# Kernel tuning notes

Hardware: AMD Instinct MI355X
Metric: run time of the kernel (lower is better)

Reference implementation:

```python
import jax, jax.numpy as jnp
import numpy as np

N = 50000      # nodes
H = 128        # hidden_size
RBF = 20       # edge_embedding_size
E_CHE = 400000 # chemical edges
E_VDW = 200000 # van-der-Waals edges


def _prelu(x, a):
    return jnp.where(x > 0, x, a * x)


def _mlp(x, w1, b1, a1, w2, b2, a2):
    # Linear -> PReLU -> Linear -> PReLU (PaiNN message / filter MLP)
    h = _prelu(x @ w1 + b1, a1)
    return _prelu(h @ w2 + b2, a2)


def setup_inputs() -> dict:
    key = jax.random.key(0)
    ks = list(jax.random.split(key, 64))
    it = iter(ks)
    d = {}
    d['node_scalar'] = jax.random.normal(next(it), (N, H), jnp.float32)
    d['node_vector'] = jax.random.normal(next(it), (N, 3, H), jnp.float32)
    for pfx, E in (('che', E_CHE), ('vdw', E_VDW)):
        d[pfx + '_edge'] = jax.random.randint(next(it), (E, 2), 0, N)
        d[pfx + '_edge_diff'] = jax.random.normal(next(it), (E, 3), jnp.float32)
        d[pfx + '_edge_dist'] = jax.random.uniform(next(it), (E,), jnp.float32) + 0.5  # strictly positive
        d[pfx + '_rbf_dist'] = jax.random.normal(next(it), (E, RBF), jnp.float32)
    # four 2-layer MLPs with per-layer PReLU scalar slope (torch default init 0.25)
    def mlp_params(pfx, din):
        s1 = 1.0 / np.sqrt(din)
        s2 = 1.0 / np.sqrt(H)
        d[pfx + '_w1'] = jax.random.uniform(next(it), (din, H), jnp.float32, -s1, s1)
        d[pfx + '_b1'] = jax.random.uniform(next(it), (H,), jnp.float32, -s1, s1)
        d[pfx + '_a1'] = jnp.asarray(0.25, jnp.float32)
        d[pfx + '_w2'] = jax.random.uniform(next(it), (H, 3 * H), jnp.float32, -s2, s2)
        d[pfx + '_b2'] = jax.random.uniform(next(it), (3 * H,), jnp.float32, -s2, s2)
        d[pfx + '_a2'] = jnp.asarray(0.25, jnp.float32)
    mlp_params('che_s', H)    # che scalar message MLP
    mlp_params('che_f', RBF)  # che filter layer
    mlp_params('vdw_s', H)
    mlp_params('vdw_f', RBF)
    return d


def _branch(node_scalar, node_vector, edge, edge_diff, edge_dist, rbf, sp, fp):
    # sp/fp: 6-tuples of MLP params. edge[:,1]=source gather, edge[:,0]=dest scatter.
    scalar_out = _mlp(node_scalar, *sp)          # [N, 3H]
    filter_w = _mlp(rbf, *fp)                    # [E, 3H]
    filter_out = scalar_out[edge[:, 1]] * filter_w  # gather + gate
    gate_vector, message_scalar, gate_edge = jnp.split(filter_out, 3, axis=1)
    state_vector = node_vector[edge[:, 1]] * gate_vector[:, None, :]        # [E,3,H]
    unit = edge_diff / edge_dist[:, None]                                    # [E,3]
    edge_vector = unit[:, :, None] * gate_edge[:, None, :]                   # [E,3,H]
    message_vector = state_vector + edge_vector
    res_scalar = jax.ops.segment_sum(message_scalar, edge[:, 0], num_segments=N)
    res_vector = jax.ops.segment_sum(message_vector, edge[:, 0], num_segments=N)
    return res_scalar, res_vector


def reference(node_scalar, node_vector,
              che_edge, che_edge_diff, che_edge_dist, che_rbf_dist,
              vdw_edge, vdw_edge_diff, vdw_edge_dist, vdw_rbf_dist,
              che_s_w1, che_s_b1, che_s_a1, che_s_w2, che_s_b2, che_s_a2,
              che_f_w1, che_f_b1, che_f_a1, che_f_w2, che_f_b2, che_f_a2,
              vdw_s_w1, vdw_s_b1, vdw_s_a1, vdw_s_w2, vdw_s_b2, vdw_s_a2,
              vdw_f_w1, vdw_f_b1, vdw_f_a1, vdw_f_w2, vdw_f_b2, vdw_f_a2):
    che_sp = (che_s_w1, che_s_b1, che_s_a1, che_s_w2, che_s_b2, che_s_a2)
    che_fp = (che_f_w1, che_f_b1, che_f_a1, che_f_w2, che_f_b2, che_f_a2)
    vdw_sp = (vdw_s_w1, vdw_s_b1, vdw_s_a1, vdw_s_w2, vdw_s_b2, vdw_s_a2)
    vdw_fp = (vdw_f_w1, vdw_f_b1, vdw_f_a1, vdw_f_w2, vdw_f_b2, vdw_f_a2)
    che_rs, che_rv = _branch(node_scalar, node_vector, che_edge, che_edge_diff,
                             che_edge_dist, che_rbf_dist, che_sp, che_fp)
    vdw_rs, vdw_rv = _branch(node_scalar, node_vector, vdw_edge, vdw_edge_diff,
                             vdw_edge_dist, vdw_rbf_dist, vdw_sp, vdw_fp)
    return (node_scalar + che_rs + vdw_rs, node_vector + che_rv + vdw_rv)
```

## Files before the change

kernel.cpp:

```cpp
#include <hip/hip_runtime.h>
#include <hip/hip_bf16.h>

typedef float f32x4 __attribute__((ext_vector_type(4)));
typedef short bf16x8 __attribute__((ext_vector_type(8)));

#define HD 128
#define TILE 32
#define SCAN_TILE 2048

__device__ __forceinline__ float prelu_f(float x, float a) {
  return x > 0.f ? x : a * x;
}

__device__ __forceinline__ unsigned short f2bf(float x) {
  __hip_bfloat16 h = __float2bfloat16(x);
  return *reinterpret_cast<unsigned short*>(&h);
}
__device__ __forceinline__ float bf2f(unsigned short u) {
  union { unsigned u; float f; } a; a.u = ((unsigned)u) << 16;
  return a.f;
}
__device__ __forceinline__ f32x4 bf4_to_f32(ushort4 u) {
  f32x4 r; r[0] = bf2f(u.x); r[1] = bf2f(u.y); r[2] = bf2f(u.z); r[3] = bf2f(u.w);
  return r;
}

__global__ __launch_bounds__(256) void init_conv_kernel(
    const f32x4* __restrict__ ns, const f32x4* __restrict__ nv,
    f32x4* __restrict__ out, ushort4* __restrict__ ns_bf, ushort4* __restrict__ nv_bf,
    int n_ns4, int n_nv4)
{
  int total = n_ns4 + n_nv4;
  for (int i = blockIdx.x * 256 + threadIdx.x; i < total; i += gridDim.x * 256) {
    f32x4 v = (i < n_ns4) ? ns[i] : nv[i - n_ns4];
    out[i] = v;
    ushort4 o;
    o.x = f2bf(v[0]); o.y = f2bf(v[1]); o.z = f2bf(v[2]); o.w = f2bf(v[3]);
    if (i < n_ns4) ns_bf[i] = o; else nv_bf[i - n_ns4] = o;
  }
}

__global__ __launch_bounds__(256) void weights_prep_kernel(
    const float* __restrict__ w2s_che, const float* __restrict__ w2f_che,
    const float* __restrict__ w2s_vdw, const float* __restrict__ w2f_vdw,
    const float* __restrict__ w1n_che, const float* __restrict__ w1n_vdw,
    const float* __restrict__ w1e_che, const float* __restrict__ w1e_vdw,
    unsigned short* __restrict__ d_w2t_sche, unsigned short* __restrict__ d_w2t_fche,
    unsigned short* __restrict__ d_w2t_svdw, unsigned short* __restrict__ d_w2t_fvdw,
    unsigned short* __restrict__ d_w1t_nche, unsigned short* __restrict__ d_w1t_nvdw,
    unsigned short* __restrict__ d_w1t_eche, unsigned short* __restrict__ d_w1t_evdw)
{
  int idx = blockIdx.x * 256 + threadIdx.x;
  if (idx < 4 * 49152) {
    int which = idx / 49152, rem = idx % 49152;
    int c = rem >> 7, k = rem & 127;
    const float* s = which == 0 ? w2s_che : which == 1 ? w2f_che : which == 2 ? w2s_vdw : w2f_vdw;
    unsigned short* d = which == 0 ? d_w2t_sche : which == 1 ? d_w2t_fche : which == 2 ? d_w2t_svdw : d_w2t_fvdw;
    d[rem] = f2bf(s[(size_t)k * 384 + c]);
  } else if (idx < 4 * 49152 + 2 * 16384) {
    int rem2 = idx - 4 * 49152;
    int which = rem2 / 16384, rem = rem2 % 16384;
    int c = rem >> 7, k = rem & 127;
    const float* s = which ? w1n_vdw : w1n_che;
    unsigned short* d = which ? d_w1t_nvdw : d_w1t_nche;
    d[rem] = f2bf(s[(size_t)k * 128 + c]);
  } else if (idx < 4 * 49152 + 2 * 16384 + 2 * 4096) {
    int rem2 = idx - 4 * 49152 - 2 * 16384;
    int which = rem2 / 4096, rem = rem2 % 4096;
    int c = rem >> 5, k = rem & 31;
    const float* s = which ? w1e_vdw : w1e_che;
    unsigned short* d = which ? d_w1t_evdw : d_w1t_eche;
    d[rem] = (k < 20) ? f2bf(s[(size_t)k * 128 + c]) : (unsigned short)0;
  }
}

__global__ __launch_bounds__(256) void node_mlp_mfma(
    const unsigned short* __restrict__ Abf,
    const unsigned short* __restrict__ w1t,
    const float* __restrict__ b1, const float* __restrict__ a1p,
    const unsigned short* __restrict__ w2t,
    const float* __restrict__ b2, const float* __restrict__ a2p,
    unsigned short* __restrict__ out,
    int M)
{
  __shared__ __attribute__((aligned(16))) unsigned short A_lds[64 * HD];
  __shared__ __attribute__((aligned(16))) unsigned short h_lds[64 * HD];
  const int t = threadIdx.x;
  const int wvid = t >> 6, lane = t & 63, l15 = lane & 15, l4 = lane >> 4;
  const int m0 = blockIdx.x * 64;
  const float a1 = a1p[0], a2 = a2p[0];

  for (int idx = t; idx < 64 * HD / 8; idx += 256) {
    int row = idx >> 4, seg = (idx & 15) * 8;
    bf16x8 v = 0;
    if (m0 + row < M) v = *(const bf16x8*)&Abf[(size_t)(m0 + row) * HD + seg];
    *(bf16x8*)&A_lds[row * HD + (seg ^ ((row & 7) << 3))] = v;
  }
  __syncthreads();

  {
    bf16x8 Bf[2][4];
    #pragma unroll
    for (int nf = 0; nf < 2; nf++)
      #pragma unroll
      for (int ks = 0; ks < 4; ks++) {
        int col = wvid * 32 + nf * 16 + l15;
        Bf[nf][ks] = *(const bf16x8*)&w1t[(size_t)col * 128 + ks * 32 + l4 * 8];
      }
    f32x4 D[4][2];
    #pragma unroll
    for (int mi = 0; mi < 4; mi++)
      #pragma unroll
      for (int nf = 0; nf < 2; nf++)
        #pragma unroll
        for (int cc = 0; cc < 4; cc++) D[mi][nf][cc] = 0.f;

    #pragma unroll
    for (int mi = 0; mi < 4; mi++)
      #pragma unroll
      for (int ks = 0; ks < 4; ks++) {
        int row = mi * 16 + l15;
        bf16x8 Af = *(const bf16x8*)&A_lds[row * HD + ((ks * 32 + l4 * 8) ^ ((row & 7) << 3))];
        D[mi][0] = __builtin_amdgcn_mfma_f32_16x16x32_bf16(Af, Bf[0][ks], D[mi][0], 0, 0, 0);
        D[mi][1] = __builtin_amdgcn_mfma_f32_16x16x32_bf16(Af, Bf[1][ks], D[mi][1], 0, 0, 0);
      }

    float b1v0 = b1[wvid * 32 + l15];
    float b1v1 = b1[wvid * 32 + 16 + l15];
    #pragma unroll
    for (int mi = 0; mi < 4; mi++)
      #pragma unroll
      for (int nf = 0; nf < 2; nf++)
        #pragma unroll
        for (int r4 = 0; r4 < 4; r4++) {
          int row = mi * 16 + l4 * 4 + r4;
          int col = wvid * 32 + nf * 16 + l15;
          h_lds[row * HD + (col ^ ((row & 7) << 3))] =
              f2bf(prelu_f(D[mi][nf][r4] + (nf ? b1v1 : b1v0), a1));
        }
  }
  __syncthreads();

  for (int m = 0; m < 3; m++) {
    bf16x8 Bf[2][4];
    #pragma unroll
    for (int nf = 0; nf < 2; nf++)
      #pragma unroll
      for (int ks = 0; ks < 4; ks++) {
        int col = m * 128 + wvid * 32 + nf * 16 + l15;
        Bf[nf][ks] = *(const bf16x8*)&w2t[(size_t)col * 128 + ks * 32 + l4 * 8];
      }
    f32x4 D[4][2];
    #pragma unroll
    for (int mi = 0; mi < 4; mi++)
      #pragma unroll
      for (int nf = 0; nf < 2; nf++)
        #pragma unroll
        for (int cc = 0; cc < 4; cc++) D[mi][nf][cc] = 0.f;

    #pragma unroll
    for (int mi = 0; mi < 4; mi++)
      #pragma unroll
      for (int ks = 0; ks < 4; ks++) {
        int row = mi * 16 + l15;
        bf16x8 Af = *(const bf16x8*)&h_lds[row * HD + ((ks * 32 + l4 * 8) ^ ((row & 7) << 3))];
        D[mi][0] = __builtin_amdgcn_mfma_f32_16x16x32_bf16(Af, Bf[0][ks], D[mi][0], 0, 0, 0);
        D[mi][1] = __builtin_amdgcn_mfma_f32_16x16x32_bf16(Af, Bf[1][ks], D[mi][1], 0, 0, 0);
      }

    float b2v0 = b2[m * 128 + wvid * 32 + l15];
    float b2v1 = b2[m * 128 + wvid * 32 + 16 + l15];
    #pragma unroll
    for (int mi = 0; mi < 4; mi++)
      #pragma unroll
      for (int nf = 0; nf < 2; nf++)
        #pragma unroll
        for (int r4 = 0; r4 < 4; r4++) {
          int row = mi * 16 + l4 * 4 + r4;
          if (m0 + row < M) {
            int col = m * 128 + wvid * 32 + nf * 16 + l15;
            out[(size_t)(m0 + row) * 384 + col] =
                f2bf(prelu_f(D[mi][nf][r4] + (nf ? b2v1 : b2v0), a2));
          }
        }
  }
}

__global__ __launch_bounds__(256) void zero_int_kernel(int* __restrict__ p, int n) {
  int i = blockIdx.x * 256 + threadIdx.x;
  if (i < n) p[i] = 0;
}

__global__ __launch_bounds__(256) void hist2_kernel(
    const int* __restrict__ edge_che, const int* __restrict__ edge_vdw,
    int* __restrict__ counts, int N, int E_che, int E_vdw)
{
  int g = blockIdx.x * 256 + threadIdx.x;
  if (g < E_che) {
    atomicAdd(&counts[edge_che[(size_t)g * 2]], 1);
  } else {
    int e2 = g - E_che;
    if (e2 < E_vdw) atomicAdd(&counts[N + edge_vdw[(size_t)e2 * 2]], 1);
  }
}

__global__ __launch_bounds__(256) void scan_partial2_kernel(
    const int* __restrict__ counts, int* __restrict__ partials, int n, int nb)
{
  const int b = blockIdx.x, t = threadIdx.x;
  const int br = b >= nb, lb = b - br * nb;
  const int* cnt = counts + (size_t)br * n;
  const int base = lb * SCAN_TILE + t * 8;
  int s = 0;
  #pragma unroll
  for (int i = 0; i < 8; i++) {
    int idx = base + i;
    if (idx < n) s += cnt[idx];
  }
  __shared__ int sums[256];
  sums[t] = s;
  __syncthreads();
  for (int o = 128; o > 0; o >>= 1) {
    if (t < o) sums[t] += sums[t + o];
    __syncthreads();
  }
  if (t == 0) partials[b] = sums[0];
}

__global__ __launch_bounds__(256) void scan_partials2_kernel(int* __restrict__ partials_g, int nb)
{
  int* partials = partials_g + blockIdx.x * nb;
  __shared__ int s[256];
  const int t = threadIdx.x;
  s[t] = (t < nb) ? partials[t] : 0;
  __syncthreads();
  for (int o = 1; o < 256; o <<= 1) {
    int v = s[t];
    int u = (t >= o) ? s[t - o] : 0;
    __syncthreads();
    s[t] = v + u;
    __syncthreads();
  }
  if (t < nb) partials[t] = (t == 0) ? 0 : s[t - 1];
}

__global__ __launch_bounds__(256) void scan_write2_kernel(
    const int* __restrict__ counts, const int* __restrict__ partials,
    int* __restrict__ offsets, int* __restrict__ cursor, int n, int nb,
    int E_che, int E_vdw)
{
  const int b = blockIdx.x, t = threadIdx.x;
  const int br = b >= nb, lb = b - br * nb;
  const int* cnt = counts + (size_t)br * n;
  int* offs = offsets + (size_t)br * (n + 1);
  int* curs = cursor + (size_t)br * n;
  const int base = lb * SCAN_TILE + t * 8;
  int vals[8];
  int s = 0;
  #pragma unroll
  for (int i = 0; i < 8; i++) {
    int idx = base + i;
    vals[i] = (idx < n) ? cnt[idx] : 0;
    s += vals[i];
  }
  __shared__ int sums[256];
  sums[t] = s;
  __syncthreads();
  for (int o = 1; o < 256; o <<= 1) {
    int v = sums[t];
    int u = (t >= o) ? sums[t - o] : 0;
    __syncthreads();
    sums[t] = v + u;
    __syncthreads();
  }
  int run = partials[b] + ((t == 0) ? 0 : sums[t - 1]);
  #pragma unroll
  for (int i = 0; i < 8; i++) {
    int idx = base + i;
    if (idx < n) {
      offs[idx] = run;
      curs[idx] = run;
      run += vals[i];
    }
  }
  if (lb == 0 && t == 0) offs[n] = br ? E_vdw : E_che;
}

__global__ __launch_bounds__(256) void scatter_ids2_kernel(
    const int* __restrict__ edge_che, const int* __restrict__ edge_vdw,
    int* __restrict__ cursor, int* __restrict__ edge_list,
    int N, int E_che, int E_vdw)
{
  int g = blockIdx.x * 256 + threadIdx.x;
  if (g < E_che) {
    int d = edge_che[(size_t)g * 2];
    int p = atomicAdd(&cursor[d], 1);
    edge_list[p] = g;
  } else {
    int e2 = g - E_che;
    if (e2 < E_vdw) {
      int d = edge_vdw[(size_t)e2 * 2];
      int p = atomicAdd(&cursor[N + d], 1);
      edge_list[E_che + p] = e2;
    }
  }
}

__global__ __launch_bounds__(256) void permute2_kernel(
    const int* __restrict__ edge_list,
    const int* __restrict__ edge_che, const float* __restrict__ diff_che,
    const float* __restrict__ dist_che, const float* __restrict__ rbf_che,
    const int* __restrict__ edge_vdw, const float* __restrict__ diff_vdw,
    const float* __restrict__ dist_vdw, const float* __restrict__ rbf_vdw,
    int* __restrict__ src_s, int* __restrict__ dst_s,
    float4* __restrict__ unit_s, unsigned short* __restrict__ rbf_b,
    int E_che, int E_vdw)
{
  int p = blockIdx.x * 256 + threadIdx.x;
  if (p >= E_che + E_vdw) return;
  int br = p >= E_che;
  int e = edge_list[p];
  const int* edge = br ? edge_vdw : edge_che;
  const float* diff = br ? diff_vdw : diff_che;
  const float* dist = br ? dist_vdw : dist_che;
  const float* rbf  = br ? rbf_vdw  : rbf_che;
  src_s[p] = edge[(size_t)e * 2 + 1];
  dst_s[p] = edge[(size_t)e * 2 + 0];
  float inv = 1.f / dist[e];
  float4 u;
  u.x = diff[(size_t)e * 3 + 0] * inv;
  u.y = diff[(size_t)e * 3 + 1] * inv;
  u.z = diff[(size_t)e * 3 + 2] * inv;
  u.w = 0.f;
  unit_s[p] = u;
  ushort4* ro = (ushort4*)(rbf_b + (size_t)p * 32);
  const float* rr = &rbf[(size_t)e * 20];
  #pragma unroll
  for (int i = 0; i < 5; i++) {
    ushort4 o;
    o.x = f2bf(rr[4 * i + 0]); o.y = f2bf(rr[4 * i + 1]);
    o.z = f2bf(rr[4 * i + 2]); o.w = f2bf(rr[4 * i + 3]);
    ro[i] = o;
  }
  ushort4 z; z.x = 0; z.y = 0; z.z = 0; z.w = 0;
  ro[5] = z; ro[6] = z; ro[7] = z;
}

__global__ __launch_bounds__(256, 4) void edge_mfma_reduce_kernel(
    const unsigned short* __restrict__ so,
    const unsigned short* __restrict__ nv,
    const int*   __restrict__ src_s,
    const int*   __restrict__ dst_s,
    const float4* __restrict__ unit_s,
    const unsigned short* __restrict__ rbf_b,
    const int*   __restrict__ offsets,
    const unsigned short* __restrict__ w1t,
    const float* __restrict__ b1, const float* __restrict__ a1p,
    const unsigned short* __restrict__ w2t,
    const float* __restrict__ b2, const float* __restrict__ a2p,
    float* __restrict__ out,
    int N, int E)
{
  __shared__ __attribute__((aligned(16))) unsigned short A1_lds[TILE * 40];
  __shared__ __attribute__((aligned(16))) unsigned short h_lds[TILE * HD];
  __shared__ __attribute__((aligned(16))) unsigned short P_lds[3][TILE * HD];
  __shared__ int src_l[TILE];
  __shared__ float unit_l[TILE][3];
  __shared__ int run_rs[TILE + 1], run_node[TILE], run_flag[TILE];
  __shared__ int nd_s;

  const int t = threadIdx.x;
  const int tx = t & 31, ty = t >> 5;
  const int c4 = tx * 4;
  const int wvid = t >> 6, lane = t & 63, l15 = lane & 15, l4 = lane >> 4;
  const int pblk = blockIdx.x * TILE;
  const int nrows = min(TILE, E - pblk);
  const float a1 = a1p[0], a2 = a2p[0];

  if (t < 64) {
    int d = -1, s = 0;
    float ux = 0.f, uy = 0.f, uz = 0.f;
    if (t < nrows) {
      s = src_s[pblk + t];
      d = dst_s[pblk + t];
      float4 u = unit_s[pblk + t];
      ux = u.x; uy = u.y; uz = u.z;
    }
    if (t < TILE) {
      src_l[t] = s;
      unit_l[t][0] = ux; unit_l[t][1] = uy; unit_l[t][2] = uz;
    }
    int dprev = __shfl_up(d, 1);
    bool flag = (t < nrows) && (t == 0 || d != dprev);
    unsigned long long mask = __ballot(flag ? 1 : 0);
    if (flag) {
      int j = __popcll(mask & ((1ull << t) - 1ull));
      run_rs[j] = t;
      run_node[j] = d;
      unsigned long long rest = (t == 63) ? 0ull : (mask >> (t + 1));
      int re = rest ? (t + 1 + (__ffsll((long long)rest) - 1)) : nrows;
      int interior = 1;
      if (t == 0 && offsets[d] != pblk) interior = 0;
      if (re == nrows && offsets[d + 1] != pblk + nrows) interior = 0;
      run_flag[j] = interior;
    }
    if (t == 0) {
      int nd = __popcll(mask);
      nd_s = nd;
      run_rs[nd] = nrows;
    }
  }

  if (t < TILE * 4) {
    const bf16x8* rb = (const bf16x8*)(rbf_b + (size_t)pblk * 32);
    int row = t >> 2, seg = (t & 3) * 8;
    *(bf16x8*)&A1_lds[row * 40 + seg] = rb[t];
  }
  __syncthreads();

  {
    bf16x8 B1[2];
    B1[0] = *(const bf16x8*)&w1t[(size_t)(wvid * 32 + l15) * 32 + l4 * 8];
    B1[1] = *(const bf16x8*)&w1t[(size_t)(wvid * 32 + 16 + l15) * 32 + l4 * 8];
    f32x4 D1[2][2];
    #pragma unroll
    for (int mi = 0; mi < 2; mi++)
      #pragma unroll
      for (int nf = 0; nf < 2; nf++)
        #pragma unroll
        for (int cc = 0; cc < 4; cc++) D1[mi][nf][cc] = 0.f;

    #pragma unroll
    for (int mi = 0; mi < 2; mi++) {
      bf16x8 Af = *(const bf16x8*)&A1_lds[(mi * 16 + l15) * 40 + l4 * 8];
      D1[mi][0] = __builtin_amdgcn_mfma_f32_16x16x32_bf16(Af, B1[0], D1[mi][0], 0, 0, 0);
      D1[mi][1] = __builtin_amdgcn_mfma_f32_16x16x32_bf16(Af, B1[1], D1[mi][1], 0, 0, 0);
    }

    float b1v0 = b1[wvid * 32 + l15];
    float b1v1 = b1[wvid * 32 + 16 + l15];
    #pragma unroll
    for (int mi = 0; mi < 2; mi++)
      #pragma unroll
      for (int nf = 0; nf < 2; nf++)
        #pragma unroll
        for (int r4 = 0; r4 < 4; r4++) {
          int row = mi * 16 + l4 * 4 + r4;
          int col = wvid * 32 + nf * 16 + l15;
          h_lds[row * HD + (col ^ ((row & 7) << 3))] =
              f2bf(prelu_f(D1[mi][nf][r4] + (nf ? b1v1 : b1v0), a1));
        }
  }
  __syncthreads();

  for (int m = 0; m < 3; m++) {
    bf16x8 Bf[2][4];
    #pragma unroll
    for (int nf = 0; nf < 2; nf++)
      #pragma unroll
      for (int ks = 0; ks < 4; ks++) {
        int col = m * 128 + wvid * 32 + nf * 16 + l15;
        Bf[nf][ks] = *(const bf16x8*)&w2t[(size_t)col * 128 + ks * 32 + l4 * 8];
      }
    f32x4 D[2][2];
    #pragma unroll
    for (int mi = 0; mi < 2; mi++)
      #pragma unroll
      for (int nf = 0; nf < 2; nf++)
        #pragma unroll
        for (int cc = 0; cc < 4; cc++) D[mi][nf][cc] = 0.f;

    #pragma unroll
    for (int mi = 0; mi < 2; mi++)
      #pragma unroll
      for (int ks = 0; ks < 4; ks++) {
        int row = mi * 16 + l15;
        bf16x8 Af = *(const bf16x8*)&h_lds[row * HD + ((ks * 32 + l4 * 8) ^ ((row & 7) << 3))];
        D[mi][0] = __builtin_amdgcn_mfma_f32_16x16x32_bf16(Af, Bf[0][ks], D[mi][0], 0, 0, 0);
        D[mi][1] = __builtin_amdgcn_mfma_f32_16x16x32_bf16(Af, Bf[1][ks], D[mi][1], 0, 0, 0);
      }

    float b2v0 = b2[m * 128 + wvid * 32 + l15];
    float b2v1 = b2[m * 128 + wvid * 32 + 16 + l15];
    #pragma unroll
    for (int mi = 0; mi < 2; mi++)
      #pragma unroll
      for (int nf = 0; nf < 2; nf++)
        #pragma unroll
        for (int r4 = 0; r4 < 4; r4++) {
          int row = mi * 16 + l4 * 4 + r4;
          int col = wvid * 32 + nf * 16 + l15;
          float v = prelu_f(D[mi][nf][r4] + (nf ? b2v1 : b2v0), a2);
          P_lds[m][row * HD + (col ^ ((row & 7) << 3))] = f2bf(v);
        }
  }
  __syncthreads();

  #pragma unroll
  for (int rr = 0; rr < 4; rr++) {
    const int r = ty * 4 + rr;
    const int src = src_l[r];
    const int sc = c4 ^ ((r & 7) << 3);
    f32x4 gvp = bf4_to_f32(*(const ushort4*)&P_lds[0][r * HD + sc]);
    f32x4 msp = bf4_to_f32(*(const ushort4*)&P_lds[1][r * HD + sc]);
    f32x4 gep = bf4_to_f32(*(const ushort4*)&P_lds[2][r * HD + sc]);
    const size_t sb = (size_t)src * 384;
    f32x4 s0 = bf4_to_f32(*(const ushort4*)&so[sb + c4]);
    f32x4 s1 = bf4_to_f32(*(const ushort4*)&so[sb + HD + c4]);
    f32x4 s2 = bf4_to_f32(*(const ushort4*)&so[sb + 2 * HD + c4]);
    f32x4 v0 = bf4_to_f32(*(const ushort4*)&nv[sb + c4]);
    f32x4 v1 = bf4_to_f32(*(const ushort4*)&nv[sb + HD + c4]);
    f32x4 v2 = bf4_to_f32(*(const ushort4*)&nv[sb + 2 * HD + c4]);
    const float u0 = unit_l[r][0], u1 = unit_l[r][1], u2 = unit_l[r][2];
    ushort4 msw, m0w, m1w, m2w;
    #pragma unroll
    for (int cc = 0; cc < 4; cc++) {
      float gv = gvp[cc] * s0[cc];
      float ms = msp[cc] * s1[cc];
      float ge = gep[cc] * s2[cc];
      float mv0 = v0[cc] * gv + u0 * ge;
      float mv1 = v1[cc] * gv + u1 * ge;
      float mv2 = v2[cc] * gv + u2 * ge;
      ((unsigned short*)&msw)[cc] = f2bf(ms);
      ((unsigned short*)&m0w)[cc] = f2bf(mv0);
      ((unsigned short*)&m1w)[cc] = f2bf(mv1);
      ((unsigned short*)&m2w)[cc] = f2bf(mv2);
    }
    *(ushort4*)&h_lds[r * HD + sc]    = msw;
    *(ushort4*)&P_lds[0][r * HD + sc] = m0w;
    *(ushort4*)&P_lds[1][r * HD + sc] = m1w;
    *(ushort4*)&P_lds[2][r * HD + sc] = m2w;
  }
  __syncthreads();

  {
    const int pl = t >> 6;
    const int c2 = (t & 63) * 2;
    const unsigned short* region = (pl == 0) ? h_lds : &P_lds[pl - 1][0];
    float* out_v = out + (size_t)N * HD;
    const int nd = nd_s;
    for (int j = 0; j < nd; j++) {
      const int rs = run_rs[j], re = run_rs[j + 1];
      const int n = run_node[j];
      float a0 = 0.f, a1v = 0.f;
      for (int r = rs; r < re; r++) {
        int ad = r * HD + (((c2 & ~3) ^ ((r & 7) << 3)) | (c2 & 3));
        unsigned int u = *(const unsigned int*)&region[ad];
        a0  += bf2f((unsigned short)(u & 0xffffu));
        a1v += bf2f((unsigned short)(u >> 16));
      }
      float* dstp = (pl == 0) ? (out + (size_t)n * HD + c2)
                              : (out_v + (size_t)n * 384 + (size_t)(pl - 1) * HD + c2);
      if (run_flag[j]) {
        float2 cur = *(float2*)dstp;
        cur.x += a0; cur.y += a1v;
        *(float2*)dstp = cur;
      } else {
        atomicAdd(dstp, a0);
        atomicAdd(dstp + 1, a1v);
      }
    }
  }
}

extern "C" void kernel_launch(void* const* d_in, const int* in_sizes, int n_in,
                              void* d_out, int out_size, void* d_ws, size_t ws_size,
                              hipStream_t stream)
{
  const float* node_scalar = (const float*)d_in[0];
  const float* node_vector = (const float*)d_in[1];
  const int*   che_edge = (const int*)d_in[2];
  const float* che_diff = (const float*)d_in[3];
  const float* che_dist = (const float*)d_in[4];
  const float* che_rbf  = (const float*)d_in[5];
  const int*   vdw_edge = (const int*)d_in[6];
  const float* vdw_diff = (const float*)d_in[7];
  const float* vdw_dist = (const float*)d_in[8];
  const float* vdw_rbf  = (const float*)d_in[9];
  const float* mlp_p[24];
  for (int i = 0; i < 24; i++) mlp_p[i] = (const float*)d_in[10 + i];

  const int N = in_sizes[0] / HD;
  const int E_che = in_sizes[4];
  const int E_vdw = in_sizes[8];
  const int E_sum = E_che + E_vdw;
  const int nb_scan = (N + SCAN_TILE - 1) / SCAN_TILE;

  char* wp = (char*)d_ws;
  size_t off = 0;
  unsigned short* so_bf = (unsigned short*)(wp + off); off += (size_t)N * 384 * 2;
  unsigned short* nv_bf = (unsigned short*)(wp + off); off += (size_t)N * 384 * 2;
  unsigned short* ns_bf = (unsigned short*)(wp + off); off += (size_t)N * 128 * 2;
  int* counts     = (int*)(wp + off);   off += (size_t)2 * N * 4;
  int* cursor     = (int*)(wp + off);   off += (size_t)2 * N * 4;
  int* offsets    = (int*)(wp + off);   off += (size_t)2 * (N + 1) * 4;
  int* partials   = (int*)(wp + off);   off += 512 * 4;
  off = (off + 255) & ~(size_t)255;
  int* edge_list  = (int*)(wp + off);   off += (size_t)E_sum * 4;
  int* src_s      = (int*)(wp + off);   off += (size_t)E_sum * 4;
  int* dst_s      = (int*)(wp + off);   off += (size_t)E_sum * 4;
  off = (off + 255) & ~(size_t)255;
  float4* unit_s  = (float4*)(wp + off); off += (size_t)E_sum * 16;
  unsigned short* rbf_b = (unsigned short*)(wp + off); off += (size_t)E_sum * 64;
  off = (off + 255) & ~(size_t)255;
  unsigned short* w2t_sche = (unsigned short*)(wp + off); off += 384 * 128 * 2;
  unsigned short* w2t_fche = (unsigned short*)(wp + off); off += 384 * 128 * 2;
  unsigned short* w2t_svdw = (unsigned short*)(wp + off); off += 384 * 128 * 2;
  unsigned short* w2t_fvdw = (unsigned short*)(wp + off); off += 384 * 128 * 2;
  unsigned short* w1t_nche = (unsigned short*)(wp + off); off += 128 * 128 * 2;
  unsigned short* w1t_nvdw = (unsigned short*)(wp + off); off += 128 * 128 * 2;
  unsigned short* w1t_eche = (unsigned short*)(wp + off); off += 128 * 32 * 2;
  unsigned short* w1t_evdw = (unsigned short*)(wp + off); off += 128 * 32 * 2;

  const int n_ns4 = N * HD / 4;
  const int n_nv4 = N * 3 * HD / 4;
  init_conv_kernel<<<2048, 256, 0, stream>>>(
      (const f32x4*)node_scalar, (const f32x4*)node_vector, (f32x4*)d_out,
      (ushort4*)ns_bf, (ushort4*)nv_bf, n_ns4, n_nv4);

  weights_prep_kernel<<<928, 256, 0, stream>>>(
      mlp_p[3], mlp_p[9], mlp_p[15], mlp_p[21],
      mlp_p[0], mlp_p[12], mlp_p[6], mlp_p[18],
      w2t_sche, w2t_fche, w2t_svdw, w2t_fvdw,
      w1t_nche, w1t_nvdw, w1t_eche, w1t_evdw);

  zero_int_kernel<<<(2 * N + 255) / 256, 256, 0, stream>>>(counts, 2 * N);
  hist2_kernel<<<(E_sum + 255) / 256, 256, 0, stream>>>(
      che_edge, vdw_edge, counts, N, E_che, E_vdw);
  scan_partial2_kernel<<<2 * nb_scan, 256, 0, stream>>>(counts, partials, N, nb_scan);
  scan_partials2_kernel<<<2, 256, 0, stream>>>(partials, nb_scan);
  scan_write2_kernel<<<2 * nb_scan, 256, 0, stream>>>(
      counts, partials, offsets, cursor, N, nb_scan, E_che, E_vdw);
  scatter_ids2_kernel<<<(E_sum + 255) / 256, 256, 0, stream>>>(
      che_edge, vdw_edge, cursor, edge_list, N, E_che, E_vdw);
  permute2_kernel<<<(E_sum + 255) / 256, 256, 0, stream>>>(
      edge_list,
      che_edge, che_diff, che_dist, che_rbf,
      vdw_edge, vdw_diff, vdw_dist, vdw_rbf,
      src_s, dst_s, unit_s, rbf_b, E_che, E_vdw);

  for (int br = 0; br < 2; br++) {
    const int E = br == 0 ? E_che : E_vdw;
    const int base = br == 0 ? 0 : E_che;
    const float* const* sp = &mlp_p[br == 0 ? 0 : 12];
    const float* const* fp = &mlp_p[br == 0 ? 6 : 18];
    const unsigned short* w2t_s = br == 0 ? w2t_sche : w2t_svdw;
    const unsigned short* w2t_f = br == 0 ? w2t_fche : w2t_fvdw;
    const unsigned short* w1t_n = br == 0 ? w1t_nche : w1t_nvdw;
    const unsigned short* w1t_e = br == 0 ? w1t_eche : w1t_evdw;

    node_mlp_mfma<<<(N + 63) / 64, 256, 0, stream>>>(
        ns_bf, w1t_n, sp[1], sp[2], w2t_s, sp[4], sp[5], so_bf, N);

    edge_mfma_reduce_kernel<<<(E + TILE - 1) / TILE, 256, 0, stream>>>(
        so_bf, nv_bf,
        src_s + base, dst_s + base, unit_s + base, rbf_b + (size_t)base * 32,
        offsets + (size_t)br * (N + 1),
        w1t_e, fp[1], fp[2], w2t_f, fp[4], fp[5],
        (float*)d_out, N, E);
  }
}
```

Before: 628.7 us.

## Merge chemical and vdW edge branches into one destination-sorted edge kernel

Sorts both edge sets jointly by destination node and processes them in a single edge kernel, tagging each edge with its branch bit. The first filter layer uses a concatenated block-diagonal weight on a 64-wide padded RBF input. The second layer runs both weight sets and keeps the result matching each row's branch. This reduces per-node scatter runs and atomics and removes a launch, at the cost of doubled layer-2 MFMA work and doubled RBF storage.

```diff
diff --git a/kernel.cpp b/kernel.cpp
--- a/kernel.cpp
+++ b/kernel.cpp
@@ -48,7 +48,7 @@
     unsigned short* __restrict__ d_w2t_sche, unsigned short* __restrict__ d_w2t_fche,
     unsigned short* __restrict__ d_w2t_svdw, unsigned short* __restrict__ d_w2t_fvdw,
     unsigned short* __restrict__ d_w1t_nche, unsigned short* __restrict__ d_w1t_nvdw,
-    unsigned short* __restrict__ d_w1t_eche, unsigned short* __restrict__ d_w1t_evdw)
+    unsigned short* __restrict__ d_w1cat)
 {
   int idx = blockIdx.x * 256 + threadIdx.x;
   if (idx < 4 * 49152) {
@@ -64,13 +64,13 @@
     const float* s = which ? w1n_vdw : w1n_che;
     unsigned short* d = which ? d_w1t_nvdw : d_w1t_nche;
     d[rem] = f2bf(s[(size_t)k * 128 + c]);
-  } else if (idx < 4 * 49152 + 2 * 16384 + 2 * 4096) {
-    int rem2 = idx - 4 * 49152 - 2 * 16384;
-    int which = rem2 / 4096, rem = rem2 % 4096;
-    int c = rem >> 5, k = rem & 31;
-    const float* s = which ? w1e_vdw : w1e_che;
-    unsigned short* d = which ? d_w1t_evdw : d_w1t_eche;
-    d[rem] = (k < 20) ? f2bf(s[(size_t)k * 128 + c]) : (unsigned short)0;
+  } else if (idx < 4 * 49152 + 2 * 16384 + 128 * 64) {
+    int rem = idx - 4 * 49152 - 2 * 16384;
+    int c = rem >> 6, k = rem & 63;
+    unsigned short v = 0;
+    if (k < 20)                v = f2bf(w1e_che[(size_t)k * 128 + c]);
+    else if (k >= 32 && k < 52) v = f2bf(w1e_vdw[(size_t)(k - 32) * 128 + c]);
+    d_w1cat[rem] = v;
   }
 }
 
@@ -191,31 +191,32 @@
   if (i < n) p[i] = 0;
 }
 
-__global__ __launch_bounds__(256) void hist2_kernel(
+__global__ __launch_bounds__(256) void hist_m_kernel(
     const int* __restrict__ edge_che, const int* __restrict__ edge_vdw,
-    int* __restrict__ counts, int N, int E_che, int E_vdw)
+    int* __restrict__ counts_che, int* __restrict__ counts_tot,
+    int E_che, int E_vdw)
 {
   int g = blockIdx.x * 256 + threadIdx.x;
   if (g < E_che) {
-    atomicAdd(&counts[edge_che[(size_t)g * 2]], 1);
+    int d = edge_che[(size_t)g * 2];
+    atomicAdd(&counts_che[d], 1);
+    atomicAdd(&counts_tot[d], 1);
   } else {
     int e2 = g - E_che;
-    if (e2 < E_vdw) atomicAdd(&counts[N + edge_vdw[(size_t)e2 * 2]], 1);
-  }
-}
-
-__global__ __launch_bounds__(256) void scan_partial2_kernel(
-    const int* __restrict__ counts, int* __restrict__ partials, int n, int nb)
+    if (e2 < E_vdw) atomicAdd(&counts_tot[edge_vdw[(size_t)e2 * 2]], 1);
+  }
+}
+
+__global__ __launch_bounds__(256) void scan_partial_kernel(
+    const int* __restrict__ counts, int* __restrict__ partials, int n)
 {
   const int b = blockIdx.x, t = threadIdx.x;
-  const int br = b >= nb, lb = b - br * nb;
-  const int* cnt = counts + (size_t)br * n;
-  const int base = lb * SCAN_TILE + t * 8;
+  const int base = b * SCAN_TILE + t * 8;
   int s = 0;
   #pragma unroll
   for (int i = 0; i < 8; i++) {
     int idx = base + i;
-    if (idx < n) s += cnt[idx];
+    if (idx < n) s += counts[idx];
   }
   __shared__ int sums[256];
   sums[t] = s;
@@ -227,9 +228,8 @@
   if (t == 0) partials[b] = sums[0];
 }
 
-__global__ __launch_bounds__(256) void scan_partials2_kernel(int* __restrict__ partials_g, int nb)
-{
-  int* partials = partials_g + blockIdx.x * nb;
+__global__ __launch_bounds__(256) void scan_partials_kernel(int* __restrict__ partials, int nb)
+{
   __shared__ int s[256];
   const int t = threadIdx.x;
   s[t] = (t < nb) ? partials[t] : 0;
@@ -244,23 +244,20 @@
   if (t < nb) partials[t] = (t == 0) ? 0 : s[t - 1];
 }
 
-__global__ __launch_bounds__(256) void scan_write2_kernel(
-    const int* __restrict__ counts, const int* __restrict__ partials,
-    int* __restrict__ offsets, int* __restrict__ cursor, int n, int nb,
-    int E_che, int E_vdw)
+__global__ __launch_bounds__(256) void scan_write_m_kernel(
+    const int* __restrict__ counts_tot, const int* __restrict__ counts_che,
+    const int* __restrict__ partials,
+    int* __restrict__ offsets, int* __restrict__ cur_che, int* __restrict__ cur_vdw,
+    int n, int E_sum)
 {
   const int b = blockIdx.x, t = threadIdx.x;
-  const int br = b >= nb, lb = b - br * nb;
-  const int* cnt = counts + (size_t)br * n;
-  int* offs = offsets + (size_t)br * (n + 1);
-  int* curs = cursor + (size_t)br * n;
-  const int base = lb * SCAN_TILE + t * 8;
+  const int base = b * SCAN_TILE + t * 8;
   int vals[8];
   int s = 0;
   #pragma unroll
   for (int i = 0; i < 8; i++) {
     int idx = base + i;
-    vals[i] = (idx < n) ? cnt[idx] : 0;
+    vals[i] = (idx < n) ? counts_tot[idx] : 0;
     s += vals[i];
   }
   __shared__ int sums[256];
@@ -278,53 +275,55 @@
   for (int i = 0; i < 8; i++) {
     int idx = base + i;
     if (idx < n) {
-      offs[idx] = run;
-      curs[idx] = run;
+      offsets[idx] = run;
+      cur_che[idx] = run;
+      cur_vdw[idx] = run + counts_che[idx];
       run += vals[i];
     }
   }
-  if (lb == 0 && t == 0) offs[n] = br ? E_vdw : E_che;
-}
-
-__global__ __launch_bounds__(256) void scatter_ids2_kernel(
+  if (b == 0 && t == 0) offsets[n] = E_sum;
+}
+
+__global__ __launch_bounds__(256) void scatter_ids_m_kernel(
     const int* __restrict__ edge_che, const int* __restrict__ edge_vdw,
-    int* __restrict__ cursor, int* __restrict__ edge_list,
-    int N, int E_che, int E_vdw)
+    int* __restrict__ cur_che, int* __restrict__ cur_vdw,
+    int* __restrict__ edge_list, int E_che, int E_vdw)
 {
   int g = blockIdx.x * 256 + threadIdx.x;
   if (g < E_che) {
     int d = edge_che[(size_t)g * 2];
-    int p = atomicAdd(&cursor[d], 1);
+    int p = atomicAdd(&cur_che[d], 1);
     edge_list[p] = g;
   } else {
     int e2 = g - E_che;
     if (e2 < E_vdw) {
       int d = edge_vdw[(size_t)e2 * 2];
-      int p = atomicAdd(&cursor[N + d], 1);
-      edge_list[E_che + p] = e2;
-    }
-  }
-}
-
-__global__ __launch_bounds__(256) void permute2_kernel(
+      int p = atomicAdd(&cur_vdw[d], 1);
+      edge_list[p] = e2 | (int)0x80000000;
+    }
+  }
+}
+
+__global__ __launch_bounds__(256) void permute_m_kernel(
     const int* __restrict__ edge_list,
     const int* __restrict__ edge_che, const float* __restrict__ diff_che,
     const float* __restrict__ dist_che, const float* __restrict__ rbf_che,
     const int* __restrict__ edge_vdw, const float* __restrict__ diff_vdw,
     const float* __restrict__ dist_vdw, const float* __restrict__ rbf_vdw,
-    int* __restrict__ src_s, int* __restrict__ dst_s,
+    int* __restrict__ srcbr_s, int* __restrict__ dst_s,
     float4* __restrict__ unit_s, unsigned short* __restrict__ rbf_b,
-    int E_che, int E_vdw)
+    int E_sum)
 {
   int p = blockIdx.x * 256 + threadIdx.x;
-  if (p >= E_che + E_vdw) return;
-  int br = p >= E_che;
-  int e = edge_list[p];
+  if (p >= E_sum) return;
+  int tag = edge_list[p];
+  int br = (int)(((unsigned)tag) >> 31);
+  int e = tag & 0x7fffffff;
   const int* edge = br ? edge_vdw : edge_che;
   const float* diff = br ? diff_vdw : diff_che;
   const float* dist = br ? dist_vdw : dist_che;
   const float* rbf  = br ? rbf_vdw  : rbf_che;
-  src_s[p] = edge[(size_t)e * 2 + 1];
+  srcbr_s[p] = edge[(size_t)e * 2 + 1] | (br << 31);
   dst_s[p] = edge[(size_t)e * 2 + 0];
   float inv = 1.f / dist[e];
   float4 u;
@@ -333,38 +332,45 @@
   u.z = diff[(size_t)e * 3 + 2] * inv;
   u.w = 0.f;
   unit_s[p] = u;
-  ushort4* ro = (ushort4*)(rbf_b + (size_t)p * 32);
+  ushort4* base = (ushort4*)(rbf_b + (size_t)p * 64);
   const float* rr = &rbf[(size_t)e * 20];
+  ushort4 z; z.x = 0; z.y = 0; z.z = 0; z.w = 0;
+  int own = br ? 8 : 0, oth = br ? 0 : 8;
   #pragma unroll
   for (int i = 0; i < 5; i++) {
     ushort4 o;
     o.x = f2bf(rr[4 * i + 0]); o.y = f2bf(rr[4 * i + 1]);
     o.z = f2bf(rr[4 * i + 2]); o.w = f2bf(rr[4 * i + 3]);
-    ro[i] = o;
-  }
-  ushort4 z; z.x = 0; z.y = 0; z.z = 0; z.w = 0;
-  ro[5] = z; ro[6] = z; ro[7] = z;
-}
-
-__global__ __launch_bounds__(256, 4) void edge_mfma_reduce_kernel(
-    const unsigned short* __restrict__ so,
+    base[own + i] = o;
+  }
+  base[own + 5] = z; base[own + 6] = z; base[own + 7] = z;
+  #pragma unroll
+  for (int i = 0; i < 8; i++) base[oth + i] = z;
+}
+
+__global__ __launch_bounds__(256, 4) void edge_merged_kernel(
+    const unsigned short* __restrict__ so_che,
+    const unsigned short* __restrict__ so_vdw,
     const unsigned short* __restrict__ nv,
-    const int*   __restrict__ src_s,
+    const int*   __restrict__ srcbr_s,
     const int*   __restrict__ dst_s,
     const float4* __restrict__ unit_s,
     const unsigned short* __restrict__ rbf_b,
     const int*   __restrict__ offsets,
-    const unsigned short* __restrict__ w1t,
-    const float* __restrict__ b1, const float* __restrict__ a1p,
-    const unsigned short* __restrict__ w2t,
-    const float* __restrict__ b2, const float* __restrict__ a2p,
+    const unsigned short* __restrict__ w1cat,
+    const float* __restrict__ b1c, const float* __restrict__ a1cp,
+    const float* __restrict__ b1v, const float* __restrict__ a1vp,
+    const unsigned short* __restrict__ w2tc,
+    const float* __restrict__ b2c, const float* __restrict__ a2cp,
+    const unsigned short* __restrict__ w2tv,
+    const float* __restrict__ b2v, const float* __restrict__ a2vp,
     float* __restrict__ out,
     int N, int E)
 {
-  __shared__ __attribute__((aligned(16))) unsigned short A1_lds[TILE * 40];
+  __shared__ __attribute__((aligned(16))) unsigned short A1_lds[TILE * 72];
   __shared__ __attribute__((aligned(16))) unsigned short h_lds[TILE * HD];
   __shared__ __attribute__((aligned(16))) unsigned short P_lds[3][TILE * HD];
-  __shared__ int src_l[TILE];
+  __shared__ int src_l[TILE], br_l[TILE];
   __shared__ float unit_l[TILE][3];
   __shared__ int run_rs[TILE + 1], run_node[TILE], run_flag[TILE];
   __shared__ int nd_s;
@@ -375,19 +381,20 @@
   const int wvid = t >> 6, lane = t & 63, l15 = lane & 15, l4 = lane >> 4;
   const int pblk = blockIdx.x * TILE;
   const int nrows = min(TILE, E - pblk);
-  const float a1 = a1p[0], a2 = a2p[0];
+  const float a1c = a1cp[0], a1v = a1vp[0], a2c = a2cp[0], a2v = a2vp[0];
 
   if (t < 64) {
-    int d = -1, s = 0;
+    int d = -1, sb = 0;
     float ux = 0.f, uy = 0.f, uz = 0.f;
     if (t < nrows) {
-      s = src_s[pblk + t];
+      sb = srcbr_s[pblk + t];
       d = dst_s[pblk + t];
       float4 u = unit_s[pblk + t];
       ux = u.x; uy = u.y; uz = u.z;
     }
     if (t < TILE) {
-      src_l[t] = s;
+      src_l[t] = sb & 0x7fffffff;
+      br_l[t] = (int)(((unsigned)sb) >> 31);
       unit_l[t][0] = ux; unit_l[t][1] = uy; unit_l[t][2] = uz;
     }
     int dprev = __shfl_up(d, 1);
@@ -411,17 +418,30 @@
     }
   }
 
-  if (t < TILE * 4) {
-    const bf16x8* rb = (const bf16x8*)(rbf_b + (size_t)pblk * 32);
-    int row = t >> 2, seg = (t & 3) * 8;
-    *(bf16x8*)&A1_lds[row * 40 + seg] = rb[t];
-  }
-  __syncthreads();
-
   {
-    bf16x8 B1[2];
-    B1[0] = *(const bf16x8*)&w1t[(size_t)(wvid * 32 + l15) * 32 + l4 * 8];
-    B1[1] = *(const bf16x8*)&w1t[(size_t)(wvid * 32 + 16 + l15) * 32 + l4 * 8];
+    const bf16x8* rb = (const bf16x8*)(rbf_b + (size_t)pblk * 64);
+    int row = t >> 3, seg = (t & 7) * 8;
+    bf16x8 v = rb[t];
+    *(bf16x8*)&A1_lds[row * 72 + seg] = v;
+  }
+  __syncthreads();
+
+  int br_row[2][4];
+  #pragma unroll
+  for (int mi = 0; mi < 2; mi++)
+    #pragma unroll
+    for (int r4 = 0; r4 < 4; r4++)
+      br_row[mi][r4] = br_l[mi * 16 + l4 * 4 + r4];
+
+  {
+    bf16x8 B1[2][2];
+    #pragma unroll
+    for (int nf = 0; nf < 2; nf++)
+      #pragma unroll
+      for (int ks = 0; ks < 2; ks++) {
+        int col = wvid * 32 + nf * 16 + l15;
+        B1[nf][ks] = *(const bf16x8*)&w1cat[(size_t)col * 64 + ks * 32 + l4 * 8];
+      }
     f32x4 D1[2][2];
     #pragma unroll
     for (int mi = 0; mi < 2; mi++)
@@ -431,14 +451,16 @@
         for (int cc = 0; cc < 4; cc++) D1[mi][nf][cc] = 0.f;
 
     #pragma unroll
-    for (int mi = 0; mi < 2; mi++) {
-      bf16x8 Af = *(const bf16x8*)&A1_lds[(mi * 16 + l15) * 40 + l4 * 8];
-      D1[mi][0] = __builtin_amdgcn_mfma_f32_16x16x32_bf16(Af, B1[0], D1[mi][0], 0, 0, 0);
-      D1[mi][1] = __builtin_amdgcn_mfma_f32_16x16x32_bf16(Af, B1[1], D1[mi][1], 0, 0, 0);
-    }
-
-    float b1v0 = b1[wvid * 32 + l15];
-    float b1v1 = b1[wvid * 32 + 16 + l15];
+    for (int mi = 0; mi < 2; mi++)
+      #pragma unroll
+      for (int ks = 0; ks < 2; ks++) {
+        bf16x8 Af = *(const bf16x8*)&A1_lds[(mi * 16 + l15) * 72 + ks * 32 + l4 * 8];
+        D1[mi][0] = __builtin_amdgcn_mfma_f32_16x16x32_bf16(Af, B1[0][ks], D1[mi][0], 0, 0, 0);
+        D1[mi][1] = __builtin_amdgcn_mfma_f32_16x16x32_bf16(Af, B1[1][ks], D1[mi][1], 0, 0, 0);
+      }
+
+    float b1c0 = b1c[wvid * 32 + l15],      b1c1 = b1c[wvid * 32 + 16 + l15];
+    float b1v0 = b1v[wvid * 32 + l15],      b1v1 = b1v[wvid * 32 + 16 + l15];
     #pragma unroll
     for (int mi = 0; mi < 2; mi++)
       #pragma unroll
@@ -447,52 +469,63 @@
         for (int r4 = 0; r4 < 4; r4++) {
           int row = mi * 16 + l4 * 4 + r4;
           int col = wvid * 32 + nf * 16 + l15;
+          int br = br_row[mi][r4];
+          float bb = br ? (nf ? b1v1 : b1v0) : (nf ? b1c1 : b1c0);
+          float aa = br ? a1v : a1c;
           h_lds[row * HD + (col ^ ((row & 7) << 3))] =
-              f2bf(prelu_f(D1[mi][nf][r4] + (nf ? b1v1 : b1v0), a1));
+              f2bf(prelu_f(D1[mi][nf][r4] + bb, aa));
         }
   }
   __syncthreads();
 
   for (int m = 0; m < 3; m++) {
-    bf16x8 Bf[2][4];
-    #pragma unroll
-    for (int nf = 0; nf < 2; nf++)
-      #pragma unroll
-      for (int ks = 0; ks < 4; ks++) {
-        int col = m * 128 + wvid * 32 + nf * 16 + l15;
-        Bf[nf][ks] = *(const bf16x8*)&w2t[(size_t)col * 128 + ks * 32 + l4 * 8];
-      }
-    f32x4 D[2][2];
-    #pragma unroll
-    for (int mi = 0; mi < 2; mi++)
+    #pragma unroll
+    for (int s = 0; s < 2; s++) {
+      const unsigned short* w2t = s ? w2tv : w2tc;
+      bf16x8 Bf[2][4];
       #pragma unroll
       for (int nf = 0; nf < 2; nf++)
         #pragma unroll
-        for (int cc = 0; cc < 4; cc++) D[mi][nf][cc] = 0.f;
-
-    #pragma unroll
-    for (int mi = 0; mi < 2; mi++)
-      #pragma unroll
-      for (int ks = 0; ks < 4; ks++) {
-        int row = mi * 16 + l15;
-        bf16x8 Af = *(const bf16x8*)&h_lds[row * HD + ((ks * 32 + l4 * 8) ^ ((row & 7) << 3))];
-        D[mi][0] = __builtin_amdgcn_mfma_f32_16x16x32_bf16(Af, Bf[0][ks], D[mi][0], 0, 0, 0);
-        D[mi][1] = __builtin_amdgcn_mfma_f32_16x16x32_bf16(Af, Bf[1][ks], D[mi][1], 0, 0, 0);
-      }
-
-    float b2v0 = b2[m * 128 + wvid * 32 + l15];
-    float b2v1 = b2[m * 128 + wvid * 32 + 16 + l15];
-    #pragma unroll
-    for (int mi = 0; mi < 2; mi++)
-      #pragma unroll
-      for (int nf = 0; nf < 2; nf++)
-        #pragma unroll
-        for (int r4 = 0; r4 < 4; r4++) {
-          int row = mi * 16 + l4 * 4 + r4;
-          int col = wvid * 32 + nf * 16 + l15;
-          float v = prelu_f(D[mi][nf][r4] + (nf ? b2v1 : b2v0), a2);
-          P_lds[m][row * HD + (col ^ ((row & 7) << 3))] = f2bf(v);
+        for (int ks = 0; ks < 4; ks++) {
+          int col = m * 128 + wvid * 32 + nf * 16 + l15;
+          Bf[nf][ks] = *(const bf16x8*)&w2t[(size_t)col * 128 + ks * 32 + l4 * 8];
         }
+      f32x4 D[2][2];
+      #pragma unroll
+      for (int mi = 0; mi < 2; mi++)
+        #pragma unroll
+        for (int nf = 0; nf < 2; nf++)
+          #pragma unroll
+          for (int cc = 0; cc < 4; cc++) D[mi][nf][cc] = 0.f;
+
+      #pragma unroll
+      for (int mi = 0; mi < 2; mi++)
+        #pragma unroll
+        for (int ks = 0; ks < 4; ks++) {
+          int row = mi * 16 + l15;
+          bf16x8 Af = *(const bf16x8*)&h_lds[row * HD + ((ks * 32 + l4 * 8) ^ ((row & 7) << 3))];
+          D[mi][0] = __builtin_amdgcn_mfma_f32_16x16x32_bf16(Af, Bf[0][ks], D[mi][0], 0, 0, 0);
+          D[mi][1] = __builtin_amdgcn_mfma_f32_16x16x32_bf16(Af, Bf[1][ks], D[mi][1], 0, 0, 0);
+        }
+
+      const float* b2 = s ? b2v : b2c;
+      float b20 = b2[m * 128 + wvid * 32 + l15];
+      float b21 = b2[m * 128 + wvid * 32 + 16 + l15];
+      float aa = s ? a2v : a2c;
+      #pragma unroll
+      for (int mi = 0; mi < 2; mi++)
+        #pragma unroll
+        for (int nf = 0; nf < 2; nf++)
+          #pragma unroll
+          for (int r4 = 0; r4 < 4; r4++) {
+            if (br_row[mi][r4] == s) {
+              int row = mi * 16 + l4 * 4 + r4;
+              int col = wvid * 32 + nf * 16 + l15;
+              float v = prelu_f(D[mi][nf][r4] + (nf ? b21 : b20), aa);
+              P_lds[m][row * HD + (col ^ ((row & 7) << 3))] = f2bf(v);
+            }
+          }
+    }
   }
   __syncthreads();
 
@@ -500,6 +533,7 @@
   for (int rr = 0; rr < 4; rr++) {
     const int r = ty * 4 + rr;
     const int src = src_l[r];
+    const unsigned short* so = br_l[r] ? so_vdw : so_che;
     const int sc = c4 ^ ((r & 7) << 3);
     f32x4 gvp = bf4_to_f32(*(const ushort4*)&P_lds[0][r * HD + sc]);
     f32x4 msp = bf4_to_f32(*(const ushort4*)&P_lds[1][r * HD + sc]);
@@ -542,22 +576,22 @@
     for (int j = 0; j < nd; j++) {
       const int rs = run_rs[j], re = run_rs[j + 1];
       const int n = run_node[j];
-      float a0 = 0.f, a1v = 0.f;
+      float a0 = 0.f, a1s = 0.f;
       for (int r = rs; r < re; r++) {
         int ad = r * HD + (((c2 & ~3) ^ ((r & 7) << 3)) | (c2 & 3));
         unsigned int u = *(const unsigned int*)&region[ad];
         a0  += bf2f((unsigned short)(u & 0xffffu));
-        a1v += bf2f((unsigned short)(u >> 16));
+        a1s += bf2f((unsigned short)(u >> 16));
       }
       float* dstp = (pl == 0) ? (out + (size_t)n * HD + c2)
                               : (out_v + (size_t)n * 384 + (size_t)(pl - 1) * HD + c2);
       if (run_flag[j]) {
         float2 cur = *(float2*)dstp;
-        cur.x += a0; cur.y += a1v;
+        cur.x += a0; cur.y += a1s;
         *(float2*)dstp = cur;
       } else {
         atomicAdd(dstp, a0);
-        atomicAdd(dstp + 1, a1v);
+        atomicAdd(dstp + 1, a1s);
       }
     }
   }
@@ -584,24 +618,28 @@
   const int E_che = in_sizes[4];
   const int E_vdw = in_sizes[8];
   const int E_sum = E_che + E_vdw;
+  const int E_pad = (E_sum + TILE - 1) & ~(TILE - 1);
   const int nb_scan = (N + SCAN_TILE - 1) / SCAN_TILE;
 
   char* wp = (char*)d_ws;
   size_t off = 0;
-  unsigned short* so_bf = (unsigned short*)(wp + off); off += (size_t)N * 384 * 2;
+  unsigned short* so_che_b = (unsigned short*)(wp + off); off += (size_t)N * 384 * 2;
+  unsigned short* so_vdw_b = (unsigned short*)(wp + off); off += (size_t)N * 384 * 2;
   unsigned short* nv_bf = (unsigned short*)(wp + off); off += (size_t)N * 384 * 2;
   unsigned short* ns_bf = (unsigned short*)(wp + off); off += (size_t)N * 128 * 2;
-  int* counts     = (int*)(wp + off);   off += (size_t)2 * N * 4;
-  int* cursor     = (int*)(wp + off);   off += (size_t)2 * N * 4;
-  int* offsets    = (int*)(wp + off);   off += (size_t)2 * (N + 1) * 4;
-  int* partials   = (int*)(wp + off);   off += 512 * 4;
+  int* counts_che = (int*)(wp + off);   off += (size_t)N * 4;
+  int* counts_tot = (int*)(wp + off);   off += (size_t)N * 4;
+  int* cur_che    = (int*)(wp + off);   off += (size_t)N * 4;
+  int* cur_vdw    = (int*)(wp + off);   off += (size_t)N * 4;
+  int* offsets    = (int*)(wp + off);   off += (size_t)(N + 1) * 4;
+  int* partials   = (int*)(wp + off);   off += 256 * 4;
   off = (off + 255) & ~(size_t)255;
   int* edge_list  = (int*)(wp + off);   off += (size_t)E_sum * 4;
-  int* src_s      = (int*)(wp + off);   off += (size_t)E_sum * 4;
+  int* srcbr_s    = (int*)(wp + off);   off += (size_t)E_sum * 4;
   int* dst_s      = (int*)(wp + off);   off += (size_t)E_sum * 4;
   off = (off + 255) & ~(size_t)255;
   float4* unit_s  = (float4*)(wp + off); off += (size_t)E_sum * 16;
-  unsigned short* rbf_b = (unsigned short*)(wp + off); off += (size_t)E_sum * 64;
+  unsigned short* rbf_b = (unsigned short*)(wp + off); off += (size_t)E_pad * 128;
   off = (off + 255) & ~(size_t)255;
   unsigned short* w2t_sche = (unsigned short*)(wp + off); off += 384 * 128 * 2;
   unsigned short* w2t_fche = (unsigned short*)(wp + off); off += 384 * 128 * 2;
@@ -609,8 +647,7 @@
   unsigned short* w2t_fvdw = (unsigned short*)(wp + off); off += 384 * 128 * 2;
   unsigned short* w1t_nche = (unsigned short*)(wp + off); off += 128 * 128 * 2;
   unsigned short* w1t_nvdw = (unsigned short*)(wp + off); off += 128 * 128 * 2;
-  unsigned short* w1t_eche = (unsigned short*)(wp + off); off += 128 * 32 * 2;
-  unsigned short* w1t_evdw = (unsigned short*)(wp + off); off += 128 * 32 * 2;
+  unsigned short* w1cat    = (unsigned short*)(wp + off); off += 128 * 64 * 2;
 
   const int n_ns4 = N * HD / 4;
   const int n_nv4 = N * 3 * HD / 4;
@@ -622,41 +659,33 @@
       mlp_p[3], mlp_p[9], mlp_p[15], mlp_p[21],
       mlp_p[0], mlp_p[12], mlp_p[6], mlp_p[18],
       w2t_sche, w2t_fche, w2t_svdw, w2t_fvdw,
-      w1t_nche, w1t_nvdw, w1t_eche, w1t_evdw);
-
-  zero_int_kernel<<<(2 * N + 255) / 256, 256, 0, stream>>>(counts, 2 * N);
-  hist2_kernel<<<(E_sum + 255) / 256, 256, 0, stream>>>(
-      che_edge, vdw_edge, counts, N, E_che, E_vdw);
-  scan_partial2_kernel<<<2 * nb_scan, 256, 0, stream>>>(counts, partials, N, nb_scan);
-  scan_partials2_kernel<<<2, 256, 0, stream>>>(partials, nb_scan);
-  scan_write2_kernel<<<2 * nb_scan, 256, 0, stream>>>(
-      counts, partials, offsets, cursor, N, nb_scan, E_che, E_vdw);
-  scatter_ids2_kernel<<<(E_sum + 255) / 256, 256, 0, stream>>>(
-      che_edge, vdw_edge, cursor, edge_list, N, E_che, E_vdw);
-  permute2_kernel<<<(E_sum + 255) / 256, 256, 0, stream>>>(
+      w1t_nche, w1t_nvdw, w1cat);
+
+  zero_int_kernel<<<(2 * N + 255) / 256, 256, 0, stream>>>(counts_che, 2 * N);
+  hist_m_kernel<<<(E_sum + 255) / 256, 256, 0, stream>>>(
+      che_edge, vdw_edge, counts_che, counts_tot, E_che, E_vdw);
+  scan_partial_kernel<<<nb_scan, 256, 0, stream>>>(counts_tot, partials, N);
+  scan_partials_kernel<<<1, 256, 0, stream>>>(partials, nb_scan);
+  scan_write_m_kernel<<<nb_scan, 256, 0, stream>>>(
+      counts_tot, counts_che, partials, offsets, cur_che, cur_vdw, N, E_sum);
+  scatter_ids_m_kernel<<<(E_sum + 255) / 256, 256, 0, stream>>>(
+      che_edge, vdw_edge, cur_che, cur_vdw, edge_list, E_che, E_vdw);
+  permute_m_kernel<<<(E_sum + 255) / 256, 256, 0, stream>>>(
       edge_list,
       che_edge, che_diff, che_dist, che_rbf,
       vdw_edge, vdw_diff, vdw_dist, vdw_rbf,
-      src_s, dst_s, unit_s, rbf_b, E_che, E_vdw);
-
-  for (int br = 0; br < 2; br++) {
-    const int E = br == 0 ? E_che : E_vdw;
-    const int base = br == 0 ? 0 : E_che;
-    const float* const* sp = &mlp_p[br == 0 ? 0 : 12];
-    const float* const* fp = &mlp_p[br == 0 ? 6 : 18];
-    const unsigned short* w2t_s = br == 0 ? w2t_sche : w2t_svdw;
-    const unsigned short* w2t_f = br == 0 ? w2t_fche : w2t_fvdw;
-    const unsigned short* w1t_n = br == 0 ? w1t_nche : w1t_nvdw;
-    const unsigned short* w1t_e = br == 0 ? w1t_eche : w1t_evdw;
-
-    node_mlp_mfma<<<(N + 63) / 64, 256, 0, stream>>>(
-        ns_bf, w1t_n, sp[1], sp[2], w2t_s, sp[4], sp[5], so_bf, N);
-
-    edge_mfma_reduce_kernel<<<(E + TILE - 1) / TILE, 256, 0, stream>>>(
-        so_bf, nv_bf,
-        src_s + base, dst_s + base, unit_s + base, rbf_b + (size_t)base * 32,
-        offsets + (size_t)br * (N + 1),
-        w1t_e, fp[1], fp[2], w2t_f, fp[4], fp[5],
-        (float*)d_out, N, E);
-  }
-}
+      srcbr_s, dst_s, unit_s, rbf_b, E_sum);
+
+  node_mlp_mfma<<<(N + 63) / 64, 256, 0, stream>>>(
+      ns_bf, w1t_nche, mlp_p[1], mlp_p[2], w2t_sche, mlp_p[4], mlp_p[5], so_che_b, N);
+  node_mlp_mfma<<<(N + 63) / 64, 256, 0, stream>>>(
+      ns_bf, w1t_nvdw, mlp_p[13], mlp_p[14], w2t_svdw, mlp_p[16], mlp_p[17], so_vdw_b, N);
+
+  edge_merged_kernel<<<(E_sum + TILE - 1) / TILE, 256, 0, stream>>>(
+      so_che_b, so_vdw_b, nv_bf,
+      srcbr_s, dst_s, unit_s, rbf_b, offsets,
+      w1cat, mlp_p[7], mlp_p[8], mlp_p[19], mlp_p[20],
+      w2t_fche, mlp_p[10], mlp_p[11],
+      w2t_fvdw, mlp_p[22], mlp_p[23],
+      (float*)d_out, N, E_sum);
+}
```

Result: slower. 841.1 us (+33.8%).
